# Performance work log

Measured on AMD Instinct MI355X. Metric: run time of the kernel, lower is better.

## Reference

```python
import jax, jax.numpy as jnp
import numpy as np

B, S, D = 2, 2048, 4096
H, HD = 32, 128  # heads, head_dim
ROPE_BASE = 10000.0


def setup_inputs() -> dict:
    key = jax.random.key(0)
    k1, k2, k3 = jax.random.split(key, 3)
    positions = jnp.broadcast_to(jnp.arange(S, dtype=jnp.int64), (B, S))
    hidden_states = jax.random.normal(k1, (B, S, D), dtype=jnp.float32)
    W_qkv = jax.random.normal(k2, (D, 3 * D), dtype=jnp.float32) * (D ** -0.5)
    W_o = jax.random.normal(k3, (D, D), dtype=jnp.float32) * (D ** -0.5)
    return {"positions": positions, "hidden_states": hidden_states, "W_qkv": W_qkv, "W_o": W_o}


def _apply_rope(x, positions):
    # x: [B,S,H,HD]; neox-style rotate-half RoPE
    half = HD // 2
    inv_freq = 1.0 / (ROPE_BASE ** (jnp.arange(0, half, dtype=jnp.float32) / half))
    ang = positions.astype(jnp.float32)[..., None] * inv_freq  # [B,S,half]
    cos = jnp.cos(ang)[:, :, None, :]  # [B,S,1,half]
    sin = jnp.sin(ang)[:, :, None, :]
    x1, x2 = x[..., :half], x[..., half:]
    return jnp.concatenate([x1 * cos - x2 * sin, x2 * cos + x1 * sin], axis=-1)


def reference(positions, hidden_states, W_qkv, W_o):
    qkv = jnp.einsum('bsd,de->bse', hidden_states, W_qkv)
    q, k, v = jnp.split(qkv, 3, axis=-1)
    q = q.reshape(B, S, H, HD)
    k = k.reshape(B, S, H, HD)
    v = v.reshape(B, S, H, HD)
    q = _apply_rope(q, positions)
    k = _apply_rope(k, positions)
    scale = HD ** -0.5
    scores = jnp.einsum('bqhd,bkhd->bhqk', q, k) * scale
    causal = jnp.tril(jnp.ones((S, S), dtype=bool))
    scores = jnp.where(causal[None, None], scores, jnp.finfo(scores.dtype).min)
    probs = jax.nn.softmax(scores, axis=-1)
    attn = jnp.einsum('bhqk,bkhd->bqhd', probs, v).reshape(B, S, D)
    return jnp.einsum('bsd,de->bse', attn, W_o)
```

## Files before the change

kernel.cpp:

```cpp
#include <hip/hip_runtime.h>
#include <hip/hip_bf16.h>
#include <stdint.h>

typedef unsigned short u16;
typedef __attribute__((ext_vector_type(8))) short short8;
typedef __attribute__((ext_vector_type(4))) float f32x4;

__device__ __forceinline__ float bf2f(u16 u) {
  union { uint32_t i; float f; } v; v.i = ((uint32_t)u) << 16; return v.f;
}
__device__ __forceinline__ u16 f2bf(float x) {
  union { float f; uint32_t i; } v; v.f = x;
  uint32_t r = v.i + 0x7FFFu + ((v.i >> 16) & 1u);
  return (u16)(r >> 16);
}
__device__ __forceinline__ void gld16(const void* g, void* l) {
  __builtin_amdgcn_global_load_lds((const __attribute__((address_space(1))) void*)g,
                                   (__attribute__((address_space(3))) void*)l, 16, 0, 0);
}


__global__ __launch_bounds__(256) void cvt_bf16_k(const float* __restrict__ in, u16* __restrict__ out, int n) {
  int i = (blockIdx.x * 256 + threadIdx.x) * 4;
  int stride = gridDim.x * 256 * 4;
  for (; i < n; i += stride) {
    float4 v = *(const float4*)(in + i);
    ushort4 o;
    o.x = f2bf(v.x); o.y = f2bf(v.y); o.z = f2bf(v.z); o.w = f2bf(v.w);
    *(ushort4*)(out + i) = o;
  }
}

__global__ __launch_bounds__(256) void transpose_cvt_k(const float* __restrict__ W, u16* __restrict__ Wt,
                                                        int Kd, int Nd) {
  __shared__ float lds[64][68];
  int t = threadIdx.x;
  int n0 = blockIdx.x * 64, k0 = blockIdx.y * 64;
  int kr = t >> 2, cq = (t & 3) * 16;
  const float* src = W + (size_t)(k0 + kr) * Nd + n0 + cq;
  float4 a = *(const float4*)(src);
  float4 b = *(const float4*)(src + 4);
  float4 c = *(const float4*)(src + 8);
  float4 d = *(const float4*)(src + 12);
  *(float4*)&lds[kr][cq]      = a;
  *(float4*)&lds[kr][cq + 4]  = b;
  *(float4*)&lds[kr][cq + 8]  = c;
  *(float4*)&lds[kr][cq + 12] = d;
  __syncthreads();
  int rn = t >> 2, ks = (t & 3) * 16;
  u16 tmp[16];
  #pragma unroll
  for (int j = 0; j < 16; ++j) tmp[j] = f2bf(lds[ks + j][rn]);
  u16* dst = Wt + (size_t)(n0 + rn) * Kd + k0 + ks;
  *(short8*)dst       = *(short8*)tmp;
  *(short8*)(dst + 8) = *(short8*)(tmp + 8);
}

__global__ __launch_bounds__(64) void rope_table_k(const int* __restrict__ pos, float* __restrict__ tab) {
  int m = blockIdx.x, i = threadIdx.x;
  float p = (float)pos[m];
  float inv = expf(-(float)i * (9.210340371976184f / 64.0f));
  float ang = p * inv;
  float sn, cs;
  sincosf(ang, &sn, &cs);
  tab[m * 128 + i] = cs;
  tab[m * 128 + 64 + i] = sn;
}


__device__ __forceinline__ void stage_half(const u16* __restrict__ G, u16* S, int K,
                                           int tile, int half, int w, int sr, int scsw) {
  int d = tile & 1;
  int sm = half * 8 + w;
  const u16* g = G + (size_t)(sm * 16 + sr) * K + (tile << 6) + scsw;
  u16* s = S + (size_t)(d * 32 + sm * 2) * 512;
  gld16(g, s);
  gld16(g + 32, s + 512);
}

__device__ __forceinline__ short8 frag(const u16* S, int d, int sidx, int kk, int fo) {
  return *(const short8*)&S[(size_t)((d * 32 + sidx * 2 + kk) * 512) + fo];
}

template <int F32OUT>
__global__ __launch_bounds__(512) void gemm256_k(const u16* __restrict__ A, const u16* __restrict__ Bt,
                                                 void* __restrict__ Cp, int N, int K, int GX) {
  __shared__ u16 As[2 * 32 * 512];
  __shared__ u16 Bs[2 * 32 * 512];
  int lid = blockIdx.x;
  int GY = gridDim.x / GX;
  int SY = GY >> 1, SX = GX >> 2;
  int xcd = lid & 7, idx = lid >> 3;
  int ry = xcd >> 2, rx = xcd & 3;
  int bxl = idx / SY, byl = idx - bxl * SY;
  int by = ry * SY + byl, bx = rx * SX + bxl;
  int bm0 = by << 8, bn0 = bx << 8;
  int tid = threadIdx.x, w = tid >> 6, l = tid & 63;
  int wr = w >> 2, wc = w & 3;
  const u16* Ag = A + (size_t)bm0 * K;
  const u16* Bg = Bt + (size_t)bn0 * K;
  int NT = K >> 6;
  int sr = l >> 2;
  int scsw = ((l & 3) * 8) ^ ((sr & 8) ? 16 : 0);
  int fr = l & 15;
  int fo = fr * 32 + (((l >> 4) * 8) ^ ((fr & 8) ? 16 : 0));

  f32x4 acc[8][4];
  #pragma unroll
  for (int i = 0; i < 8; ++i)
    #pragma unroll
    for (int j = 0; j < 4; ++j) acc[i][j] = (f32x4){0.f, 0.f, 0.f, 0.f};

  stage_half(Ag, As, K, 0, 0, w, sr, scsw);
  stage_half(Ag, As, K, 0, 1, w, sr, scsw);
  stage_half(Bg, Bs, K, 0, 0, w, sr, scsw);
  stage_half(Bg, Bs, K, 0, 1, w, sr, scsw);
  stage_half(Ag, As, K, 1, 0, w, sr, scsw);
  asm volatile("s_waitcnt vmcnt(2)" ::: "memory");
  __builtin_amdgcn_s_barrier();
  __builtin_amdgcn_sched_barrier(0);

  for (int t = 0; t < NT; ++t) {
    int d = t & 1;
    short8 a_lo[4][2], a_hi[4][2], b_lo[2][2], b_hi[2][2];
    #pragma unroll
    for (int fm = 0; fm < 4; ++fm) {
      a_lo[fm][0] = frag(As, d, wr * 8 + fm, 0, fo);
      a_lo[fm][1] = frag(As, d, wr * 8 + fm, 1, fo);
    }
    #pragma unroll
    for (int fn = 0; fn < 2; ++fn) {
      b_lo[fn][0] = frag(Bs, d, wc * 4 + fn, 0, fo);
      b_lo[fn][1] = frag(Bs, d, wc * 4 + fn, 1, fo);
    }
    if (t + 1 < NT) stage_half(Ag, As, K, t + 1, 1, w, sr, scsw);
    __builtin_amdgcn_s_barrier();
    __builtin_amdgcn_s_setprio(1);
    #pragma unroll
    for (int fm = 0; fm < 4; ++fm)
      #pragma unroll
      for (int fn = 0; fn < 2; ++fn) {
        acc[fm][fn] = __builtin_amdgcn_mfma_f32_16x16x32_bf16(a_lo[fm][0], b_lo[fn][0], acc[fm][fn], 0, 0, 0);
        acc[fm][fn] = __builtin_amdgcn_mfma_f32_16x16x32_bf16(a_lo[fm][1], b_lo[fn][1], acc[fm][fn], 0, 0, 0);
      }
    __builtin_amdgcn_s_setprio(0);
    __builtin_amdgcn_s_barrier();
    #pragma unroll
    for (int fn = 0; fn < 2; ++fn) {
      b_hi[fn][0] = frag(Bs, d, wc * 4 + 2 + fn, 0, fo);
      b_hi[fn][1] = frag(Bs, d, wc * 4 + 2 + fn, 1, fo);
    }
    if (t + 1 < NT) stage_half(Bg, Bs, K, t + 1, 0, w, sr, scsw);
    __builtin_amdgcn_s_barrier();
    __builtin_amdgcn_s_setprio(1);
    #pragma unroll
    for (int fm = 0; fm < 4; ++fm)
      #pragma unroll
      for (int fn = 0; fn < 2; ++fn) {
        acc[fm][2 + fn] = __builtin_amdgcn_mfma_f32_16x16x32_bf16(a_lo[fm][0], b_hi[fn][0], acc[fm][2 + fn], 0, 0, 0);
        acc[fm][2 + fn] = __builtin_amdgcn_mfma_f32_16x16x32_bf16(a_lo[fm][1], b_hi[fn][1], acc[fm][2 + fn], 0, 0, 0);
      }
    __builtin_amdgcn_s_setprio(0);
    __builtin_amdgcn_s_barrier();
    #pragma unroll
    for (int fm = 0; fm < 4; ++fm) {
      a_hi[fm][0] = frag(As, d, wr * 8 + 4 + fm, 0, fo);
      a_hi[fm][1] = frag(As, d, wr * 8 + 4 + fm, 1, fo);
    }
    if (t + 1 < NT) stage_half(Bg, Bs, K, t + 1, 1, w, sr, scsw);
    __builtin_amdgcn_s_barrier();
    __builtin_amdgcn_s_setprio(1);
    #pragma unroll
    for (int fm = 0; fm < 4; ++fm)
      #pragma unroll
      for (int fn = 0; fn < 2; ++fn) {
        acc[4 + fm][2 + fn] = __builtin_amdgcn_mfma_f32_16x16x32_bf16(a_hi[fm][0], b_hi[fn][0], acc[4 + fm][2 + fn], 0, 0, 0);
        acc[4 + fm][2 + fn] = __builtin_amdgcn_mfma_f32_16x16x32_bf16(a_hi[fm][1], b_hi[fn][1], acc[4 + fm][2 + fn], 0, 0, 0);
      }
    __builtin_amdgcn_s_setprio(0);
    __builtin_amdgcn_s_barrier();
    if (t + 2 < NT) stage_half(Ag, As, K, t + 2, 0, w, sr, scsw);
    __builtin_amdgcn_s_setprio(1);
    #pragma unroll
    for (int fm = 0; fm < 4; ++fm)
      #pragma unroll
      for (int fn = 0; fn < 2; ++fn) {
        acc[4 + fm][fn] = __builtin_amdgcn_mfma_f32_16x16x32_bf16(a_hi[fm][0], b_lo[fn][0], acc[4 + fm][fn], 0, 0, 0);
        acc[4 + fm][fn] = __builtin_amdgcn_mfma_f32_16x16x32_bf16(a_hi[fm][1], b_lo[fn][1], acc[4 + fm][fn], 0, 0, 0);
      }
    __builtin_amdgcn_s_setprio(0);
    if (t + 2 < NT) asm volatile("s_waitcnt vmcnt(2)" ::: "memory");
    else            asm volatile("s_waitcnt vmcnt(0)" ::: "memory");
    __builtin_amdgcn_s_barrier();
    __builtin_amdgcn_sched_barrier(0);
  }

  int r0 = bm0 + wr * 128 + ((l >> 4) << 2);
  int c0 = bn0 + wc * 64 + (l & 15);
  #pragma unroll
  for (int fm = 0; fm < 8; ++fm)
    #pragma unroll
    for (int fn = 0; fn < 4; ++fn)
      #pragma unroll
      for (int r = 0; r < 4; ++r) {
        size_t idx2 = (size_t)(r0 + fm * 16 + r) * N + (c0 + fn * 16);
        if (F32OUT) ((float*)Cp)[idx2] = acc[fm][fn][r];
        else        ((u16*)Cp)[idx2]   = f2bf(acc[fm][fn][r]);
      }
}


__global__ __launch_bounds__(256) void rope_qk_k(const u16* __restrict__ qkv, const float* __restrict__ tab,
                                                  u16* __restrict__ Qb, u16* __restrict__ Kb) {
  int m = blockIdx.x, t = threadIdx.x;
  int b = m >> 11, s = m & 2047;
  const float* tabm = tab + m * 128;
  #pragma unroll
  for (int part = 0; part < 2; ++part) {
    const u16* src = qkv + (size_t)m * 12288 + part * 4096;
    u16* dst = part ? Kb : Qb;
    float qs = part ? 1.0f : 0.08838834764831845f;
    #pragma unroll
    for (int it = 0; it < 2; ++it) {
      int v = t + it * 256;
      int h = v >> 4;
      int d1 = (v & 15) * 4;
      const u16* sp = src + h * 128 + d1;
      ushort4 x1 = *(const ushort4*)(sp);
      ushort4 x2 = *(const ushort4*)(sp + 64);
      float4 cs = *(const float4*)(tabm + d1);
      float4 sn = *(const float4*)(tabm + 64 + d1);
      ushort4 o1, o2;
      o1.x = f2bf((bf2f(x1.x) * cs.x - bf2f(x2.x) * sn.x) * qs);
      o1.y = f2bf((bf2f(x1.y) * cs.y - bf2f(x2.y) * sn.y) * qs);
      o1.z = f2bf((bf2f(x1.z) * cs.z - bf2f(x2.z) * sn.z) * qs);
      o1.w = f2bf((bf2f(x1.w) * cs.w - bf2f(x2.w) * sn.w) * qs);
      o2.x = f2bf((bf2f(x2.x) * cs.x + bf2f(x1.x) * sn.x) * qs);
      o2.y = f2bf((bf2f(x2.y) * cs.y + bf2f(x1.y) * sn.y) * qs);
      o2.z = f2bf((bf2f(x2.z) * cs.z + bf2f(x1.z) * sn.z) * qs);
      o2.w = f2bf((bf2f(x2.w) * cs.w + bf2f(x1.w) * sn.w) * qs);
      u16* o = dst + ((size_t)(b * 32 + h) * 2048 + s) * 128 + d1;
      *(ushort4*)o        = o1;
      *(ushort4*)(o + 64) = o2;
    }
  }
}

__global__ __launch_bounds__(256) void v_transpose_k(const u16* __restrict__ qkv, u16* __restrict__ Vt) {
  __shared__ u16 lds[64][136];
  int bid = blockIdx.x;
  int bh = bid >> 5, st = bid & 31;
  int b = bh >> 5, h = bh & 31;
  int s0 = st * 64;
  int t = threadIdx.x;
  int r = t >> 2, cq = (t & 3) * 32;
  const u16* src = qkv + (size_t)(b * 2048 + s0 + r) * 12288 + 8192 + h * 128 + cq;
  *(short8*)&lds[r][cq]      = *(const short8*)(src);
  *(short8*)&lds[r][cq + 8]  = *(const short8*)(src + 8);
  *(short8*)&lds[r][cq + 16] = *(const short8*)(src + 16);
  *(short8*)&lds[r][cq + 24] = *(const short8*)(src + 24);
  __syncthreads();
  int d = t >> 1, sseg = (t & 1) * 32;
  u16 tmp[32];
  #pragma unroll
  for (int j = 0; j < 32; ++j) tmp[j] = lds[sseg + j][d];
  u16* o = Vt + (size_t)bh * (128 * 2048) + (size_t)d * 2048 + s0 + sseg;
  *(short8*)(o)      = *(short8*)(tmp);
  *(short8*)(o + 8)  = *(short8*)(tmp + 8);
  *(short8*)(o + 16) = *(short8*)(tmp + 16);
  *(short8*)(o + 24) = *(short8*)(tmp + 24);
}


__device__ __forceinline__ void stage_kv(const u16* __restrict__ Kg, const u16* __restrict__ Vg,
                                         u16* Ksb, u16* Vsb, int j0, int w, int l) {
  #pragma unroll
  for (int c = 0; c < 2; ++c) {
    int rk = c * 32 + w * 4 + (l >> 4);
    int kcol = ((l & 15) * 8) ^ ((rk & 7) << 3);
    gld16(Kg + (size_t)(j0 + rk) * 128 + kcol, Ksb + (c * 32 + w * 4) * 128);
    int rv = c * 64 + w * 8 + (l >> 3);
    int vcol = ((l & 7) * 8) ^ ((rv & 7) << 3);
    gld16(Vg + (size_t)rv * 2048 + j0 + vcol, Vsb + (c * 64 + w * 8) * 64);
  }
}

__global__ __launch_bounds__(512, 2) void attn_k(const u16* __restrict__ Qb, const u16* __restrict__ Kb,
                                                  const u16* __restrict__ Vt, u16* __restrict__ attnb) {
  __shared__ u16 Ks[2][64 * 128];
  __shared__ u16 Vs[2][128 * 64];
  __shared__ u16 Ps[8][32 * 64];
  int lid = blockIdx.x + gridDim.x * blockIdx.y;
  int xcd = lid & 7, idx = lid >> 3;
  int bh = xcd * 8 + (idx >> 3);
  int qt = idx & 7;
  int b = bh >> 5, h = bh & 31;
  int q0 = qt * 256;
  int t = threadIdx.x, w = t >> 6, l = t & 63;
  int g = l >> 4, fr = l & 15;
  const u16* Qg = Qb + (size_t)bh * (2048 * 128);
  const u16* Kg = Kb + (size_t)bh * (2048 * 128);
  const u16* Vg = Vt + (size_t)bh * (128 * 2048);

  short8 aq[2][4];
  #pragma unroll
  for (int fm = 0; fm < 2; ++fm)
    #pragma unroll
    for (int kk = 0; kk < 4; ++kk)
      aq[fm][kk] = *(const short8*)&Qg[(size_t)(q0 + w * 32 + fm * 16 + fr) * 128 + kk * 32 + g * 8];

  stage_kv(Kg, Vg, Ks[0], Vs[0], 0, w, l);
  __syncthreads();

  f32x4 zero = {0.f, 0.f, 0.f, 0.f};
  f32x4 o[2][8];
  #pragma unroll
  for (int fm = 0; fm < 2; ++fm)
    #pragma unroll
    for (int fd = 0; fd < 8; ++fd) o[fm][fd] = zero;
  float m_run[2][4], l_run[2][4];
  #pragma unroll
  for (int fm = 0; fm < 2; ++fm)
    #pragma unroll
    for (int r = 0; r < 4; ++r) { m_run[fm][r] = -1e30f; l_run[fm][r] = 0.f; }

  int NJ = 4 * qt + 4;
  for (int j = 0; j < NJ; ++j) {
    int j0 = j * 64;
    int cur = j & 1;
    if (j + 1 < NJ) stage_kv(Kg, Vg, Ks[cur ^ 1], Vs[cur ^ 1], j0 + 64, w, l);
    if (j0 < q0 + w * 32 + 32) {
      f32x4 sc[2][4];
      #pragma unroll
      for (int fm = 0; fm < 2; ++fm)
        #pragma unroll
        for (int fn = 0; fn < 4; ++fn) sc[fm][fn] = zero;
      __builtin_amdgcn_s_setprio(1);
      #pragma unroll
      for (int kk = 0; kk < 4; ++kk) {
        #pragma unroll
        for (int fn = 0; fn < 4; ++fn) {
          short8 bk = *(const short8*)&Ks[cur][(fn * 16 + fr) * 128 + ((kk * 32 + g * 8) ^ ((fr & 7) << 3))];
          #pragma unroll
          for (int fm = 0; fm < 2; ++fm)
            sc[fm][fn] = __builtin_amdgcn_mfma_f32_16x16x32_bf16(aq[fm][kk], bk, sc[fm][fn], 0, 0, 0);
        }
      }
      __builtin_amdgcn_s_setprio(0);
      int qb_ = q0 + w * 32 + (g << 2);
      int kb_ = j0 + fr;
      #pragma unroll
      for (int fm = 0; fm < 2; ++fm)
        #pragma unroll
        for (int fn = 0; fn < 4; ++fn)
          #pragma unroll
          for (int r = 0; r < 4; ++r)
            if (kb_ + fn * 16 > qb_ + fm * 16 + r) sc[fm][fn][r] = -1e30f;
      float mx[2][4];
      #pragma unroll
      for (int fm = 0; fm < 2; ++fm)
        #pragma unroll
        for (int r = 0; r < 4; ++r) {
          float v = fmaxf(fmaxf(sc[fm][0][r], sc[fm][1][r]), fmaxf(sc[fm][2][r], sc[fm][3][r]));
          v = fmaxf(v, __shfl_xor(v, 1));
          v = fmaxf(v, __shfl_xor(v, 2));
          v = fmaxf(v, __shfl_xor(v, 4));
          v = fmaxf(v, __shfl_xor(v, 8));
          mx[fm][r] = v;
        }
      float scale[2][4];
      #pragma unroll
      for (int fm = 0; fm < 2; ++fm)
        #pragma unroll
        for (int r = 0; r < 4; ++r) {
          float mn = fmaxf(m_run[fm][r], mx[fm][r]);
          scale[fm][r] = __expf(m_run[fm][r] - mn);
          m_run[fm][r] = mn;
        }
      float rs[2][4];
      #pragma unroll
      for (int fm = 0; fm < 2; ++fm)
        #pragma unroll
        for (int r = 0; r < 4; ++r) {
          float acc = 0.f;
          #pragma unroll
          for (int fn = 0; fn < 4; ++fn) {
            float p = __expf(sc[fm][fn][r] - m_run[fm][r]);
            sc[fm][fn][r] = p;
            acc += p;
          }
          acc += __shfl_xor(acc, 1);
          acc += __shfl_xor(acc, 2);
          acc += __shfl_xor(acc, 4);
          acc += __shfl_xor(acc, 8);
          rs[fm][r] = acc;
        }
      #pragma unroll
      for (int fm = 0; fm < 2; ++fm)
        #pragma unroll
        for (int r = 0; r < 4; ++r) l_run[fm][r] = l_run[fm][r] * scale[fm][r] + rs[fm][r];
      #pragma unroll
      for (int fm = 0; fm < 2; ++fm)
        #pragma unroll
        for (int fd = 0; fd < 8; ++fd)
          #pragma unroll
          for (int r = 0; r < 4; ++r) o[fm][fd][r] *= scale[fm][r];
      #pragma unroll
      for (int fm = 0; fm < 2; ++fm)
        #pragma unroll
        for (int fn = 0; fn < 4; ++fn)
          #pragma unroll
          for (int r = 0; r < 4; ++r) {
            int prow = fm * 16 + (g << 2) + r;
            Ps[w][prow * 64 + ((fn * 16 + fr) ^ ((prow & 7) << 3))] = f2bf(sc[fm][fn][r]);
          }
      __builtin_amdgcn_s_setprio(1);
      #pragma unroll
      for (int kk = 0; kk < 2; ++kk) {
        short8 pa[2];
        #pragma unroll
        for (int fm = 0; fm < 2; ++fm)
          pa[fm] = *(const short8*)&Ps[w][(fm * 16 + fr) * 64 + ((kk * 32 + g * 8) ^ ((fr & 7) << 3))];
        #pragma unroll
        for (int fd = 0; fd < 8; ++fd) {
          short8 bv = *(const short8*)&Vs[cur][(fd * 16 + fr) * 64 + ((kk * 32 + g * 8) ^ ((fr & 7) << 3))];
          #pragma unroll
          for (int fm = 0; fm < 2; ++fm)
            o[fm][fd] = __builtin_amdgcn_mfma_f32_16x16x32_bf16(pa[fm], bv, o[fm][fd], 0, 0, 0);
        }
      }
      __builtin_amdgcn_s_setprio(0);
    }
    __syncthreads();
  }

  #pragma unroll
  for (int fm = 0; fm < 2; ++fm)
    #pragma unroll
    for (int r = 0; r < 4; ++r) {
      float inv = 1.0f / l_run[fm][r];
      int srow = q0 + w * 32 + fm * 16 + (g << 2) + r;
      u16* dst = attnb + (size_t)(b * 2048 + srow) * 4096 + h * 128 + fr;
      #pragma unroll
      for (int fd = 0; fd < 8; ++fd)
        dst[fd * 16] = f2bf(o[fm][fd][r] * inv);
    }
}


extern "C" void kernel_launch(void* const* d_in, const int* in_sizes, int n_in,
                              void* d_out, int out_size, void* d_ws, size_t ws_size,
                              hipStream_t stream) {
  const int*   positions = (const int*)d_in[0];
  const float* hidden    = (const float*)d_in[1];
  const float* W_qkv     = (const float*)d_in[2];
  const float* W_o       = (const float*)d_in[3];
  float* out = (float*)d_out;
  char* ws = (char*)d_ws;

  u16* R0 = (u16*)ws;
  u16* R1 = (u16*)(ws + 100663296);
  u16* R2 = (u16*)(ws + 201326592);
  float* tab = (float*)(ws + 234881024);

  u16* hidden_bf = R2;
  u16* Wqkv_t = R0;
  u16* qkv = R1;
  u16* Qb = R2;
  u16* Kb = R0;
  u16* Vt = R0 + 16777216;
  u16* attnb = R0 + 33554432;
  u16* Wo_t = R1;

  cvt_bf16_k<<<4096, 256, 0, stream>>>(hidden, hidden_bf, 16777216);
  transpose_cvt_k<<<dim3(192, 64), 256, 0, stream>>>(W_qkv, Wqkv_t, 4096, 12288);
  rope_table_k<<<4096, 64, 0, stream>>>(positions, tab);

  gemm256_k<0><<<768, 512, 0, stream>>>(hidden_bf, Wqkv_t, qkv, 12288, 4096, 48);

  rope_qk_k<<<4096, 256, 0, stream>>>(qkv, tab, Qb, Kb);
  v_transpose_k<<<2048, 256, 0, stream>>>(qkv, Vt);
  transpose_cvt_k<<<dim3(64, 64), 256, 0, stream>>>(W_o, Wo_t, 4096, 4096);

  attn_k<<<dim3(8, 64), 512, 0, stream>>>(Qb, Kb, Vt, attnb);

  gemm256_k<1><<<256, 512, 0, stream>>>(attnb, Wo_t, out, 4096, 4096, 16);
}
```

Measured before the change: 862.0 us.

## Restructure GEMM prefetch into per-fragment-set stages with finer-grained vmcnt waits

Staging is reorganised around the fragment sets each MFMA phase consumes: A and B rows are split into two sets that match a_lo/a_hi and b_lo/b_hi. All of tile t+1 is now prefetched during iteration t, instead of keeping a partial prefetch of tile t+2. A vmcnt wait is placed before each MFMA phase, so each phase waits only for the set it needs rather than one wait at the end of the iteration. The aim is to issue global->LDS loads earlier and shorten the stall at the end of each iteration. In exchange there is more waitcnt/barrier coupling, and the prefetch distance is shallower.

```diff
diff --git a/kernel.cpp b/kernel.cpp
--- a/kernel.cpp
+++ b/kernel.cpp
@@ -68,10 +68,12 @@
 }
 
 
-__device__ __forceinline__ void stage_half(const u16* __restrict__ G, u16* S, int K,
-                                           int tile, int half, int w, int sr, int scsw) {
+template <int ISB>
+__device__ __forceinline__ void stage_set(const u16* __restrict__ G, u16* S, int K,
+                                          int tile, int set, int w, int sr, int scsw) {
   int d = tile & 1;
-  int sm = half * 8 + w;
+  int sm = ISB ? ((w & 1) + ((w >> 1) << 2) + (set << 1))
+               : ((w & 3) + ((w >> 2) << 3) + (set << 2));
   const u16* g = G + (size_t)(sm * 16 + sr) * K + (tile << 6) + scsw;
   u16* s = S + (size_t)(d * 32 + sm * 2) * 512;
   gld16(g, s);
@@ -111,18 +113,19 @@
     #pragma unroll
     for (int j = 0; j < 4; ++j) acc[i][j] = (f32x4){0.f, 0.f, 0.f, 0.f};
 
-  stage_half(Ag, As, K, 0, 0, w, sr, scsw);
-  stage_half(Ag, As, K, 0, 1, w, sr, scsw);
-  stage_half(Bg, Bs, K, 0, 0, w, sr, scsw);
-  stage_half(Bg, Bs, K, 0, 1, w, sr, scsw);
-  stage_half(Ag, As, K, 1, 0, w, sr, scsw);
-  asm volatile("s_waitcnt vmcnt(2)" ::: "memory");
+  stage_set<0>(Ag, As, K, 0, 0, w, sr, scsw);
+  stage_set<1>(Bg, Bs, K, 0, 0, w, sr, scsw);
+  stage_set<1>(Bg, Bs, K, 0, 1, w, sr, scsw);
+  stage_set<0>(Ag, As, K, 0, 1, w, sr, scsw);
+  asm volatile("s_waitcnt vmcnt(4)" ::: "memory");
   __builtin_amdgcn_s_barrier();
   __builtin_amdgcn_sched_barrier(0);
 
   for (int t = 0; t < NT; ++t) {
     int d = t & 1;
+    bool pf = (t + 1 < NT);
     short8 a_lo[4][2], a_hi[4][2], b_lo[2][2], b_hi[2][2];
+    if (pf) stage_set<0>(Ag, As, K, t + 1, 0, w, sr, scsw);
     #pragma unroll
     for (int fm = 0; fm < 4; ++fm) {
       a_lo[fm][0] = frag(As, d, wr * 8 + fm, 0, fo);
@@ -133,7 +136,8 @@
       b_lo[fn][0] = frag(Bs, d, wc * 4 + fn, 0, fo);
       b_lo[fn][1] = frag(Bs, d, wc * 4 + fn, 1, fo);
     }
-    if (t + 1 < NT) stage_half(Ag, As, K, t + 1, 1, w, sr, scsw);
+    if (pf) asm volatile("s_waitcnt vmcnt(4)" ::: "memory");
+    else    asm volatile("s_waitcnt vmcnt(2)" ::: "memory");
     __builtin_amdgcn_s_barrier();
     __builtin_amdgcn_s_setprio(1);
     #pragma unroll
@@ -145,12 +149,14 @@
       }
     __builtin_amdgcn_s_setprio(0);
     __builtin_amdgcn_s_barrier();
+    if (pf) stage_set<1>(Bg, Bs, K, t + 1, 0, w, sr, scsw);
     #pragma unroll
     for (int fn = 0; fn < 2; ++fn) {
       b_hi[fn][0] = frag(Bs, d, wc * 4 + 2 + fn, 0, fo);
       b_hi[fn][1] = frag(Bs, d, wc * 4 + 2 + fn, 1, fo);
     }
-    if (t + 1 < NT) stage_half(Bg, Bs, K, t + 1, 0, w, sr, scsw);
+    if (pf) asm volatile("s_waitcnt vmcnt(4)" ::: "memory");
+    else    asm volatile("s_waitcnt vmcnt(0)" ::: "memory");
     __builtin_amdgcn_s_barrier();
     __builtin_amdgcn_s_setprio(1);
     #pragma unroll
@@ -162,12 +168,14 @@
       }
     __builtin_amdgcn_s_setprio(0);
     __builtin_amdgcn_s_barrier();
+    if (pf) stage_set<1>(Bg, Bs, K, t + 1, 1, w, sr, scsw);
     #pragma unroll
     for (int fm = 0; fm < 4; ++fm) {
       a_hi[fm][0] = frag(As, d, wr * 8 + 4 + fm, 0, fo);
       a_hi[fm][1] = frag(As, d, wr * 8 + 4 + fm, 1, fo);
     }
-    if (t + 1 < NT) stage_half(Bg, Bs, K, t + 1, 1, w, sr, scsw);
+    if (pf) asm volatile("s_waitcnt vmcnt(4)" ::: "memory");
+    else    asm volatile("s_waitcnt vmcnt(0)" ::: "memory");
     __builtin_amdgcn_s_barrier();
     __builtin_amdgcn_s_setprio(1);
     #pragma unroll
@@ -179,7 +187,9 @@
       }
     __builtin_amdgcn_s_setprio(0);
     __builtin_amdgcn_s_barrier();
-    if (t + 2 < NT) stage_half(Ag, As, K, t + 2, 0, w, sr, scsw);
+    if (pf) stage_set<0>(Ag, As, K, t + 1, 1, w, sr, scsw);
+    if (pf) asm volatile("s_waitcnt vmcnt(4)" ::: "memory");
+    else    asm volatile("s_waitcnt vmcnt(0)" ::: "memory");
     __builtin_amdgcn_s_setprio(1);
     #pragma unroll
     for (int fm = 0; fm < 4; ++fm)
@@ -189,8 +199,6 @@
         acc[4 + fm][fn] = __builtin_amdgcn_mfma_f32_16x16x32_bf16(a_hi[fm][1], b_lo[fn][1], acc[4 + fm][fn], 0, 0, 0);
       }
     __builtin_amdgcn_s_setprio(0);
-    if (t + 2 < NT) asm volatile("s_waitcnt vmcnt(2)" ::: "memory");
-    else            asm volatile("s_waitcnt vmcnt(0)" ::: "memory");
     __builtin_amdgcn_s_barrier();
     __builtin_amdgcn_sched_barrier(0);
   }
```

Measured after the change: 1.036 ms. 1.2x slower.
